# Kernel optimization log

Measured on AMD Instinct MI355X. Metric: run time of the kernel, lower is better.

## Reference

```python
import jax, jax.numpy as jnp
import numpy as np

N_NODES = 40000
N_EDGES = 640000
N_GRAPHS = 256


def gcn_conv(x, W, b, src, dst, deg_inv_sqrt):
    # GCNConv: D^{-1/2} (A + I) D^{-1/2} X W + b
    h = (x @ W) * deg_inv_sqrt[:, None]          # pre-scale by norm of source
    agg = jax.ops.segment_sum(h[src], dst, num_segments=x.shape[0])
    agg = agg + h                                 # self-loop contribution
    return agg * deg_inv_sqrt[:, None] + b


def setup_inputs() -> dict:
    key = jax.random.key(0)
    ks = jax.random.split(key, 12)
    x = jax.random.normal(ks[0], (N_NODES, 128), dtype=jnp.float32)
    edge_index = jax.random.randint(ks[1], (2, N_EDGES), 0, N_NODES, dtype=jnp.int64)
    batch = jnp.sort(jax.random.randint(ks[2], (N_NODES,), 0, N_GRAPHS, dtype=jnp.int64))

    def glorot(k, shape):
        lim = float(np.sqrt(6.0 / (shape[0] + shape[1])))
        return jax.random.uniform(k, shape, jnp.float32, -lim, lim)

    return {
        "x": x,
        "W1": glorot(ks[3], (128, 128)), "b1": jnp.zeros((128,), jnp.float32),
        "W2": glorot(ks[4], (128, 64)),  "b2": jnp.zeros((64,), jnp.float32),
        "W3": glorot(ks[5], (64, 32)),   "b3": jnp.zeros((32,), jnp.float32),
        "Wl": glorot(ks[6], (32, 768)),  "bl": jnp.zeros((768,), jnp.float32),
        "edge_index": edge_index,
        "batch": batch,
    }


def reference(x, W1, b1, W2, b2, W3, b3, Wl, bl, edge_index, batch):
    n = x.shape[0]
    src, dst = edge_index[0], edge_index[1]
    # degree including self-loop (PyG gcn_norm with add_self_loops=True)
    deg = jax.ops.segment_sum(jnp.ones_like(dst, dtype=x.dtype), dst, num_segments=n) + 1.0
    dis = jax.lax.rsqrt(deg)

    h = jax.nn.relu(gcn_conv(x, W1, b1, src, dst, dis))
    h = jax.nn.relu(gcn_conv(h, W2, b2, src, dst, dis))
    h = jax.nn.relu(gcn_conv(h, W3, b3, src, dst, dis))

    # global mean pool per graph
    counts = jax.ops.segment_sum(jnp.ones((n,), x.dtype), batch, num_segments=N_GRAPHS)
    pooled = jax.ops.segment_sum(h, batch, num_segments=N_GRAPHS)
    pooled = pooled / jnp.maximum(counts, 1.0)[:, None]

    out = pooled @ Wl + bl                        # [B, 768]
    return out.reshape(N_GRAPHS, 48, 16)          # [B, 3*S^2, c]
```

## Files before the change

kernel.cpp:

```cpp
#include <hip/hip_runtime.h>
#include <hip/hip_fp16.h>


struct H8 { __half2 a, b, c, d; };


__global__ void deg_count_kernel(const int* __restrict__ dst, int* __restrict__ deg, int E) {
    int e = blockIdx.x * blockDim.x + threadIdx.x;
    if (e < E) atomicAdd(&deg[dst[e]], 1);
}

__global__ void scan1_kernel(const int* __restrict__ deg, int* __restrict__ off,
                             int* __restrict__ bsums, int N) {
    __shared__ int s[256];
    const int tid = threadIdx.x;
    const int i = blockIdx.x * 256 + tid;
    const int v = (i < N) ? deg[i] : 0;
    s[tid] = v;
    __syncthreads();
    for (int o = 1; o < 256; o <<= 1) {
        int t = (tid >= o) ? s[tid - o] : 0;
        __syncthreads();
        s[tid] += t;
        __syncthreads();
    }
    if (i < N) off[i] = s[tid] - v;
    if (tid == 255) bsums[blockIdx.x] = s[255];
}

__global__ void scan2_kernel(int* __restrict__ bsums, int NB) {
    __shared__ int s[256];
    const int tid = threadIdx.x;
    const int v = (tid < NB) ? bsums[tid] : 0;
    s[tid] = v;
    __syncthreads();
    for (int o = 1; o < 256; o <<= 1) {
        int t = (tid >= o) ? s[tid - o] : 0;
        __syncthreads();
        s[tid] += t;
        __syncthreads();
    }
    if (tid < NB) bsums[tid] = s[tid] - v;
}

__global__ void scan3_kernel(int* __restrict__ off, const int* __restrict__ bsums,
                             int* __restrict__ cursor, const int* __restrict__ deg,
                             float* __restrict__ dis, int N, int E) {
    const int i = blockIdx.x * 256 + threadIdx.x;
    if (i < N) {
        const int o = off[i] + bsums[blockIdx.x];
        off[i] = o;
        cursor[i] = o;
        dis[i] = rsqrtf((float)deg[i] + 1.0f);
    }
    if (i == 0) off[N] = E;
}

__global__ void fill_csr_kernel(const int* __restrict__ src, const int* __restrict__ dst,
                                int* __restrict__ cursor, int* __restrict__ csr_src, int E) {
    int e = blockIdx.x * blockDim.x + threadIdx.x;
    if (e < E) {
        const int pos = atomicAdd(&cursor[dst[e]], 1);
        csr_src[pos] = src[e];
    }
}

template <int K, int C, int NR>
__global__ __launch_bounds__(256, 4) void gemm_scale_kernel(
        const float* __restrict__ x, const float* __restrict__ W,
        const float* __restrict__ dis, __half* __restrict__ h, int N) {
    constexpr int TC     = C / 8;
    constexpr int TN     = 256 / TC;
    constexpr int NPB    = NR * TN;
    constexpr int KSTAGE = 32;
    constexpr int XROW   = KSTAGE + 4;
    constexpr int WROW   = TC * 12;
    __shared__ float Xs[NPB * XROW];
    __shared__ float Ws[KSTAGE * WROW];

    const int tc = threadIdx.x % TC;
    const int tn = threadIdx.x / TC;
    const int c0 = tc * 8;
    const int nBase = blockIdx.x * NPB;
    const int n0 = nBase + tn * NR;

    float acc[NR][8] = {};

#pragma unroll 1
    for (int ks = 0; ks < K; ks += KSTAGE) {
        for (int idx = threadIdx.x; idx < KSTAGE * (C / 4); idx += 256) {
            const int k  = idx / (C / 4);
            const int f4 = idx % (C / 4);
            const int t  = f4 >> 1;
            const int hh = f4 & 1;
            *reinterpret_cast<float4*>(&Ws[k * WROW + t * 12 + hh * 4]) =
                *reinterpret_cast<const float4*>(&W[(size_t)(ks + k) * C + t * 8 + hh * 4]);
        }
        for (int idx = threadIdx.x; idx < NPB * (KSTAGE / 4); idx += 256) {
            const int row = idx / (KSTAGE / 4);
            const int c4  = (idx % (KSTAGE / 4)) * 4;
            const int nn  = nBase + row;
            const float4 v = (nn < N)
                ? *reinterpret_cast<const float4*>(&x[(size_t)nn * K + ks + c4])
                : float4{0.f, 0.f, 0.f, 0.f};
            *reinterpret_cast<float4*>(&Xs[row * XROW + c4]) = v;
        }
        __syncthreads();

#pragma unroll 2
        for (int k = 0; k < KSTAGE; k += 4) {
            float4 xv[NR];
#pragma unroll
            for (int i = 0; i < NR; ++i)
                xv[i] = *reinterpret_cast<const float4*>(&Xs[(tn * NR + i) * XROW + k]);
#pragma unroll
            for (int kk = 0; kk < 4; ++kk) {
                float wv[8];
                *reinterpret_cast<float4*>(&wv[0]) =
                    *reinterpret_cast<const float4*>(&Ws[(k + kk) * WROW + tc * 12]);
                *reinterpret_cast<float4*>(&wv[4]) =
                    *reinterpret_cast<const float4*>(&Ws[(k + kk) * WROW + tc * 12 + 4]);
#pragma unroll
                for (int i = 0; i < NR; ++i) {
                    const float xs = (&xv[i].x)[kk];
#pragma unroll
                    for (int j = 0; j < 8; ++j) acc[i][j] = fmaf(xs, wv[j], acc[i][j]);
                }
            }
        }
        __syncthreads();
    }

#pragma unroll
    for (int i = 0; i < NR; ++i) {
        const int nn = n0 + i;
        if (nn < N) {
            const float d = dis[nn];
            H8 o;
            o.a = __floats2half2_rn(acc[i][0] * d, acc[i][1] * d);
            o.b = __floats2half2_rn(acc[i][2] * d, acc[i][3] * d);
            o.c = __floats2half2_rn(acc[i][4] * d, acc[i][5] * d);
            o.d = __floats2half2_rn(acc[i][6] * d, acc[i][7] * d);
            *reinterpret_cast<H8*>(&h[(size_t)nn * C + c0]) = o;
        }
    }
}

__device__ inline void acc_h8(float* acc, const H8& v) {
    float2 f;
    f = __half22float2(v.a); acc[0] += f.x; acc[1] += f.y;
    f = __half22float2(v.b); acc[2] += f.x; acc[3] += f.y;
    f = __half22float2(v.c); acc[4] += f.x; acc[5] += f.y;
    f = __half22float2(v.d); acc[6] += f.x; acc[7] += f.y;
}

template <int C>
__global__ void gather_kernel(const __half* __restrict__ h, const int* __restrict__ off,
                              const int* __restrict__ csr_src, const float* __restrict__ dis,
                              const float* __restrict__ b, float* __restrict__ out, int N) {
    constexpr int CQ = C / 8;
    const long long tid = (long long)blockIdx.x * blockDim.x + threadIdx.x;
    const int node = (int)(tid / CQ);
    const int q    = (int)(tid % CQ);
    if (node >= N) return;

    const int beg = off[node];
    const int end = off[node + 1];

    float acc[8] = {};
    acc_h8(acc, *reinterpret_cast<const H8*>(&h[(size_t)node * C + q * 8]));

    int i = beg;
    for (; i + 4 <= end; i += 4) {
        const int s0 = csr_src[i];
        const int s1 = csr_src[i + 1];
        const int s2 = csr_src[i + 2];
        const int s3 = csr_src[i + 3];
        const H8 v0 = *reinterpret_cast<const H8*>(&h[(size_t)s0 * C + q * 8]);
        const H8 v1 = *reinterpret_cast<const H8*>(&h[(size_t)s1 * C + q * 8]);
        const H8 v2 = *reinterpret_cast<const H8*>(&h[(size_t)s2 * C + q * 8]);
        const H8 v3 = *reinterpret_cast<const H8*>(&h[(size_t)s3 * C + q * 8]);
        acc_h8(acc, v0); acc_h8(acc, v1); acc_h8(acc, v2); acc_h8(acc, v3);
    }
    for (; i < end; ++i) {
        const int s = csr_src[i];
        acc_h8(acc, *reinterpret_cast<const H8*>(&h[(size_t)s * C + q * 8]));
    }

    const float d = dis[node];
    float r[8];
#pragma unroll
    for (int j = 0; j < 8; ++j) {
        float v = fmaf(acc[j], d, b[q * 8 + j]);
        r[j] = v > 0.0f ? v : 0.0f;
    }
    *reinterpret_cast<float4*>(&out[(size_t)node * C + q * 8])     = *reinterpret_cast<float4*>(&r[0]);
    *reinterpret_cast<float4*>(&out[(size_t)node * C + q * 8 + 4]) = *reinterpret_cast<float4*>(&r[4]);
}

__global__ void pool_kernel(const float* __restrict__ x3, const int* __restrict__ batch,
                            float* __restrict__ pooled, float* __restrict__ counts, int N) {
    const long long tid = (long long)blockIdx.x * blockDim.x + threadIdx.x;
    const int ch = (int)(tid % 32);
    int n = (int)(tid / 32) * 8;
    if (n >= N) return;
    const int nEnd = (n + 8 < N) ? n + 8 : N;
    int g = batch[n];
    float acc = 0.0f, cnt = 0.0f;
    for (; n < nEnd; ++n) {
        const int gn = batch[n];
        if (gn != g) {
            atomicAdd(&pooled[g * 32 + ch], acc);
            if (ch == 0) atomicAdd(&counts[g], cnt);
            acc = 0.0f; cnt = 0.0f; g = gn;
        }
        acc += x3[(size_t)n * 32 + ch];
        cnt += 1.0f;
    }
    atomicAdd(&pooled[g * 32 + ch], acc);
    if (ch == 0) atomicAdd(&counts[g], cnt);
}

__global__ void head_kernel(const float* __restrict__ pooled, const float* __restrict__ counts,
                            const float* __restrict__ Wl, const float* __restrict__ bl,
                            float* __restrict__ out) {
    __shared__ float p[32];
    const int g = blockIdx.x;
    if (threadIdx.x < 32) {
        float cnt = counts[g];
        cnt = cnt < 1.0f ? 1.0f : cnt;
        p[threadIdx.x] = pooled[g * 32 + threadIdx.x] / cnt;
    }
    __syncthreads();
    const int j = threadIdx.x;
    float acc = bl[j];
#pragma unroll
    for (int k = 0; k < 32; ++k) acc = fmaf(p[k], Wl[k * 768 + j], acc);
    out[g * 768 + j] = acc;
}


extern "C" void kernel_launch(void* const* d_in, const int* in_sizes, int n_in,
                              void* d_out, int out_size, void* d_ws, size_t ws_size,
                              hipStream_t stream) {
    const float* x   = (const float*)d_in[0];
    const float* W1  = (const float*)d_in[1];
    const float* b1  = (const float*)d_in[2];
    const float* W2  = (const float*)d_in[3];
    const float* b2  = (const float*)d_in[4];
    const float* W3  = (const float*)d_in[5];
    const float* b3  = (const float*)d_in[6];
    const float* Wl  = (const float*)d_in[7];
    const float* bl  = (const float*)d_in[8];
    const int* ei    = (const int*)d_in[9];
    const int* batch = (const int*)d_in[10];

    const int N = in_sizes[0] / 128;
    const int E = in_sizes[9] / 2;
    const int G = out_size / 768;
    const int NB = (N + 255) / 256;

    const int* src = ei;
    const int* dst = ei + E;
    float* out = (float*)d_out;

    float* fws    = (float*)d_ws;
    __half* H     = (__half*)fws;
    float* A      = fws + (size_t)N * 128;
    float* Bb     = A + (size_t)N * 128;
    float* dis    = Bb + (size_t)N * 64;
    float* pooled = dis + N;
    float* counts = pooled + (size_t)G * 32;
    int* deg      = (int*)(counts + G);
    int* off      = deg + N;
    int* cursor   = off + (N + 1);
    int* bsums    = cursor + N;
    int* csr_src  = bsums + 256;

    hipMemsetAsync(deg, 0, (size_t)N * sizeof(int), stream);
    hipMemsetAsync(pooled, 0, ((size_t)G * 32 + G) * sizeof(float), stream);
    deg_count_kernel<<<(E + 255) / 256, 256, 0, stream>>>(dst, deg, E);
    scan1_kernel<<<NB, 256, 0, stream>>>(deg, off, bsums, N);
    scan2_kernel<<<1, 256, 0, stream>>>(bsums, NB);
    scan3_kernel<<<NB, 256, 0, stream>>>(off, bsums, cursor, deg, dis, N, E);
    fill_csr_kernel<<<(E + 255) / 256, 256, 0, stream>>>(src, dst, cursor, csr_src, E);

    gemm_scale_kernel<128, 128, 4><<<(N + 63) / 64, 256, 0, stream>>>(x, W1, dis, H, N);
    gather_kernel<128><<<(int)(((long long)N * 16 + 255) / 256), 256, 0, stream>>>(
        H, off, csr_src, dis, b1, A, N);

    gemm_scale_kernel<128, 64, 2><<<(N + 63) / 64, 256, 0, stream>>>(A, W2, dis, H, N);
    gather_kernel<64><<<(int)(((long long)N * 8 + 255) / 256), 256, 0, stream>>>(
        H, off, csr_src, dis, b2, Bb, N);

    gemm_scale_kernel<64, 32, 2><<<(N + 127) / 128, 256, 0, stream>>>(Bb, W3, dis, H, N);
    gather_kernel<32><<<(int)(((long long)N * 4 + 255) / 256), 256, 0, stream>>>(
        H, off, csr_src, dis, b3, A, N);

    pool_kernel<<<(int)(((long long)((N + 7) / 8) * 32 + 255) / 256), 256, 0, stream>>>(
        A, batch, pooled, counts, N);
    head_kernel<<<G, 768, 0, stream>>>(pooled, counts, Wl, bl, out);
}
```

Baseline: 270.2 us.

## Store layer activations in fp16, widen gather unroll, fuse pool and head

The gather kernels now write their ReLU outputs as fp16, and the next GEMM reads fp16 and converts to fp32 in shared memory. This halves the activation traffic between layers. The gather edge loop is unrolled from 4 to 8 so more loads are in flight. Pooling and the linear head become one kernel per graph that finds the graph's node range by binary search on the sorted batch vector. This removes the atomics, the memset and one launch, but the pooling now depends on batch being sorted and the activations carry extra rounding error.

```diff
diff --git a/kernel.cpp b/kernel.cpp
--- a/kernel.cpp
+++ b/kernel.cpp
@@ -65,9 +65,9 @@
     }
 }
 
-template <int K, int C, int NR>
+template <int K, int C, int NR, bool HALF_IN>
 __global__ __launch_bounds__(256, 4) void gemm_scale_kernel(
-        const float* __restrict__ x, const float* __restrict__ W,
+        const void* __restrict__ x_, const float* __restrict__ W,
         const float* __restrict__ dis, __half* __restrict__ h, int N) {
     constexpr int TC     = C / 8;
     constexpr int TN     = 256 / TC;
@@ -96,14 +96,38 @@
             *reinterpret_cast<float4*>(&Ws[k * WROW + t * 12 + hh * 4]) =
                 *reinterpret_cast<const float4*>(&W[(size_t)(ks + k) * C + t * 8 + hh * 4]);
         }
-        for (int idx = threadIdx.x; idx < NPB * (KSTAGE / 4); idx += 256) {
-            const int row = idx / (KSTAGE / 4);
-            const int c4  = (idx % (KSTAGE / 4)) * 4;
-            const int nn  = nBase + row;
-            const float4 v = (nn < N)
-                ? *reinterpret_cast<const float4*>(&x[(size_t)nn * K + ks + c4])
-                : float4{0.f, 0.f, 0.f, 0.f};
-            *reinterpret_cast<float4*>(&Xs[row * XROW + c4]) = v;
+        if (HALF_IN) {
+            const __half* xh = (const __half*)x_;
+            for (int idx = threadIdx.x; idx < NPB * (KSTAGE / 8); idx += 256) {
+                const int row = idx / (KSTAGE / 8);
+                const int c8  = (idx % (KSTAGE / 8)) * 8;
+                const int nn  = nBase + row;
+                float f[8];
+                if (nn < N) {
+                    const H8 v = *reinterpret_cast<const H8*>(&xh[(size_t)nn * K + ks + c8]);
+                    float2 t2;
+                    t2 = __half22float2(v.a); f[0] = t2.x; f[1] = t2.y;
+                    t2 = __half22float2(v.b); f[2] = t2.x; f[3] = t2.y;
+                    t2 = __half22float2(v.c); f[4] = t2.x; f[5] = t2.y;
+                    t2 = __half22float2(v.d); f[6] = t2.x; f[7] = t2.y;
+                } else {
+#pragma unroll
+                    for (int j = 0; j < 8; ++j) f[j] = 0.0f;
+                }
+                *reinterpret_cast<float4*>(&Xs[row * XROW + c8])     = *reinterpret_cast<float4*>(&f[0]);
+                *reinterpret_cast<float4*>(&Xs[row * XROW + c8 + 4]) = *reinterpret_cast<float4*>(&f[4]);
+            }
+        } else {
+            const float* xf = (const float*)x_;
+            for (int idx = threadIdx.x; idx < NPB * (KSTAGE / 4); idx += 256) {
+                const int row = idx / (KSTAGE / 4);
+                const int c4  = (idx % (KSTAGE / 4)) * 4;
+                const int nn  = nBase + row;
+                const float4 v = (nn < N)
+                    ? *reinterpret_cast<const float4*>(&xf[(size_t)nn * K + ks + c4])
+                    : float4{0.f, 0.f, 0.f, 0.f};
+                *reinterpret_cast<float4*>(&Xs[row * XROW + c4]) = v;
+            }
         }
         __syncthreads();
 
@@ -157,7 +181,7 @@
 template <int C>
 __global__ void gather_kernel(const __half* __restrict__ h, const int* __restrict__ off,
                               const int* __restrict__ csr_src, const float* __restrict__ dis,
-                              const float* __restrict__ b, float* __restrict__ out, int N) {
+                              const float* __restrict__ b, __half* __restrict__ out, int N) {
     constexpr int CQ = C / 8;
     const long long tid = (long long)blockIdx.x * blockDim.x + threadIdx.x;
     const int node = (int)(tid / CQ);
@@ -171,16 +195,15 @@
     acc_h8(acc, *reinterpret_cast<const H8*>(&h[(size_t)node * C + q * 8]));
 
     int i = beg;
-    for (; i + 4 <= end; i += 4) {
-        const int s0 = csr_src[i];
-        const int s1 = csr_src[i + 1];
-        const int s2 = csr_src[i + 2];
-        const int s3 = csr_src[i + 3];
-        const H8 v0 = *reinterpret_cast<const H8*>(&h[(size_t)s0 * C + q * 8]);
-        const H8 v1 = *reinterpret_cast<const H8*>(&h[(size_t)s1 * C + q * 8]);
-        const H8 v2 = *reinterpret_cast<const H8*>(&h[(size_t)s2 * C + q * 8]);
-        const H8 v3 = *reinterpret_cast<const H8*>(&h[(size_t)s3 * C + q * 8]);
-        acc_h8(acc, v0); acc_h8(acc, v1); acc_h8(acc, v2); acc_h8(acc, v3);
+    for (; i + 8 <= end; i += 8) {
+        int s[8];
+#pragma unroll
+        for (int u = 0; u < 8; ++u) s[u] = csr_src[i + u];
+        H8 v[8];
+#pragma unroll
+        for (int u = 0; u < 8; ++u) v[u] = *reinterpret_cast<const H8*>(&h[(size_t)s[u] * C + q * 8]);
+#pragma unroll
+        for (int u = 0; u < 8; ++u) acc_h8(acc, v[u]);
     }
     for (; i < end; ++i) {
         const int s = csr_src[i];
@@ -194,49 +217,56 @@
         float v = fmaf(acc[j], d, b[q * 8 + j]);
         r[j] = v > 0.0f ? v : 0.0f;
     }
-    *reinterpret_cast<float4*>(&out[(size_t)node * C + q * 8])     = *reinterpret_cast<float4*>(&r[0]);
-    *reinterpret_cast<float4*>(&out[(size_t)node * C + q * 8 + 4]) = *reinterpret_cast<float4*>(&r[4]);
-}
-
-__global__ void pool_kernel(const float* __restrict__ x3, const int* __restrict__ batch,
-                            float* __restrict__ pooled, float* __restrict__ counts, int N) {
-    const long long tid = (long long)blockIdx.x * blockDim.x + threadIdx.x;
-    const int ch = (int)(tid % 32);
-    int n = (int)(tid / 32) * 8;
-    if (n >= N) return;
-    const int nEnd = (n + 8 < N) ? n + 8 : N;
-    int g = batch[n];
-    float acc = 0.0f, cnt = 0.0f;
-    for (; n < nEnd; ++n) {
-        const int gn = batch[n];
-        if (gn != g) {
-            atomicAdd(&pooled[g * 32 + ch], acc);
-            if (ch == 0) atomicAdd(&counts[g], cnt);
-            acc = 0.0f; cnt = 0.0f; g = gn;
-        }
-        acc += x3[(size_t)n * 32 + ch];
-        cnt += 1.0f;
-    }
-    atomicAdd(&pooled[g * 32 + ch], acc);
-    if (ch == 0) atomicAdd(&counts[g], cnt);
-}
-
-__global__ void head_kernel(const float* __restrict__ pooled, const float* __restrict__ counts,
-                            const float* __restrict__ Wl, const float* __restrict__ bl,
-                            float* __restrict__ out) {
+    H8 o;
+    o.a = __floats2half2_rn(r[0], r[1]);
+    o.b = __floats2half2_rn(r[2], r[3]);
+    o.c = __floats2half2_rn(r[4], r[5]);
+    o.d = __floats2half2_rn(r[6], r[7]);
+    *reinterpret_cast<H8*>(&out[(size_t)node * C + q * 8]) = o;
+}
+
+__global__ __launch_bounds__(256) void poolhead_kernel(
+        const __half* __restrict__ x3, const int* __restrict__ batch,
+        const float* __restrict__ Wl, const float* __restrict__ bl,
+        float* __restrict__ out, int N) {
+    const int g = blockIdx.x;
+    __shared__ int bounds[2];
+    if (threadIdx.x == 0) {
+        int lo = 0, hi = N;
+        while (lo < hi) { int m = (lo + hi) >> 1; if (batch[m] <  g) lo = m + 1; else hi = m; }
+        bounds[0] = lo;
+        int lo2 = lo, hi2 = N;
+        while (lo2 < hi2) { int m = (lo2 + hi2) >> 1; if (batch[m] <= g) lo2 = m + 1; else hi2 = m; }
+        bounds[1] = lo2;
+    }
+    __syncthreads();
+    const int lo = bounds[0], hi = bounds[1];
+
+    const int ch  = threadIdx.x & 31;
+    const int grp = threadIdx.x >> 5;
+    float acc = 0.0f;
+    for (int n = lo + grp; n < hi; n += 8)
+        acc += __half2float(x3[(size_t)n * 32 + ch]);
+
+    __shared__ float red[8][33];
+    red[grp][ch] = acc;
+    __syncthreads();
     __shared__ float p[32];
-    const int g = blockIdx.x;
-    if (threadIdx.x < 32) {
-        float cnt = counts[g];
+    if (grp == 0) {
+        float s = red[0][ch] + red[1][ch] + red[2][ch] + red[3][ch]
+                + red[4][ch] + red[5][ch] + red[6][ch] + red[7][ch];
+        float cnt = (float)(hi - lo);
         cnt = cnt < 1.0f ? 1.0f : cnt;
-        p[threadIdx.x] = pooled[g * 32 + threadIdx.x] / cnt;
-    }
-    __syncthreads();
-    const int j = threadIdx.x;
-    float acc = bl[j];
-#pragma unroll
-    for (int k = 0; k < 32; ++k) acc = fmaf(p[k], Wl[k * 768 + j], acc);
-    out[g * 768 + j] = acc;
+        p[ch] = s / cnt;
+    }
+    __syncthreads();
+
+    for (int j = threadIdx.x; j < 768; j += 256) {
+        float a = bl[j];
+#pragma unroll
+        for (int k = 0; k < 32; ++k) a = fmaf(p[k], Wl[k * 768 + j], a);
+        out[g * 768 + j] = a;
+    }
 }
 
 
@@ -264,40 +294,34 @@
     const int* dst = ei + E;
     float* out = (float*)d_out;
 
-    float* fws    = (float*)d_ws;
-    __half* H     = (__half*)fws;
-    float* A      = fws + (size_t)N * 128;
-    float* Bb     = A + (size_t)N * 128;
-    float* dis    = Bb + (size_t)N * 64;
-    float* pooled = dis + N;
-    float* counts = pooled + (size_t)G * 32;
-    int* deg      = (int*)(counts + G);
+    __half* H     = (__half*)d_ws;
+    __half* A     = H + (size_t)N * 128;
+    __half* Bb    = A + (size_t)N * 128;
+    float* dis    = (float*)(Bb + (size_t)N * 64);
+    int* deg      = (int*)(dis + N);
     int* off      = deg + N;
     int* cursor   = off + (N + 1);
     int* bsums    = cursor + N;
     int* csr_src  = bsums + 256;
 
     hipMemsetAsync(deg, 0, (size_t)N * sizeof(int), stream);
-    hipMemsetAsync(pooled, 0, ((size_t)G * 32 + G) * sizeof(float), stream);
     deg_count_kernel<<<(E + 255) / 256, 256, 0, stream>>>(dst, deg, E);
     scan1_kernel<<<NB, 256, 0, stream>>>(deg, off, bsums, N);
     scan2_kernel<<<1, 256, 0, stream>>>(bsums, NB);
     scan3_kernel<<<NB, 256, 0, stream>>>(off, bsums, cursor, deg, dis, N, E);
     fill_csr_kernel<<<(E + 255) / 256, 256, 0, stream>>>(src, dst, cursor, csr_src, E);
 
-    gemm_scale_kernel<128, 128, 4><<<(N + 63) / 64, 256, 0, stream>>>(x, W1, dis, H, N);
+    gemm_scale_kernel<128, 128, 4, false><<<(N + 63) / 64, 256, 0, stream>>>(x, W1, dis, H, N);
     gather_kernel<128><<<(int)(((long long)N * 16 + 255) / 256), 256, 0, stream>>>(
         H, off, csr_src, dis, b1, A, N);
 
-    gemm_scale_kernel<128, 64, 2><<<(N + 63) / 64, 256, 0, stream>>>(A, W2, dis, H, N);
+    gemm_scale_kernel<128, 64, 2, true><<<(N + 63) / 64, 256, 0, stream>>>(A, W2, dis, H, N);
     gather_kernel<64><<<(int)(((long long)N * 8 + 255) / 256), 256, 0, stream>>>(
         H, off, csr_src, dis, b2, Bb, N);
 
-    gemm_scale_kernel<64, 32, 2><<<(N + 127) / 128, 256, 0, stream>>>(Bb, W3, dis, H, N);
+    gemm_scale_kernel<64, 32, 2, true><<<(N + 127) / 128, 256, 0, stream>>>(Bb, W3, dis, H, N);
     gather_kernel<32><<<(int)(((long long)N * 4 + 255) / 256), 256, 0, stream>>>(
         H, off, csr_src, dis, b3, A, N);
 
-    pool_kernel<<<(int)(((long long)((N + 7) / 8) * 32 + 255) / 256), 256, 0, stream>>>(
-        A, batch, pooled, counts, N);
-    head_kernel<<<G, 768, 0, stream>>>(pooled, counts, Wl, bl, out);
-}
+    poolhead_kernel<<<G, 256, 0, stream>>>(A, batch, Wl, bl, out, N);
+}
```

After: 269.0 us. Within noise of the previous version (-0.4%).
